# Kernel tuning notes

Measured on AMD Instinct MI355X. Metric: run time of the kernel, lower is better.

## Reference

```python
import jax, jax.numpy as jnp
import numpy as np

V = 4096      # num codes (vocab)
D = 128       # embedding dim
K = 3         # diffusion scales
H = 4         # attn heads
FF = 128      # ff hidden
L = 2         # attn layers
NVIS = 8192   # visits
MAXC = 32     # max codes per visit
PAD = 0


def logmap0(x):
    # Poincare ball (c=1) log map at origin: artanh(||x||) * x / ||x||
    eps = 1e-7
    norm = jnp.linalg.norm(x, axis=-1, keepdims=True)
    norm_c = jnp.clip(norm, eps, 1.0 - 1e-5)
    return jnp.arctanh(norm_c) * x / jnp.maximum(norm, eps)


def layer_norm(x, g, b, eps=1e-5):
    m = jnp.mean(x, axis=-1, keepdims=True)
    v = jnp.mean((x - m) ** 2, axis=-1, keepdims=True)
    return (x - m) * jax.lax.rsqrt(v + eps) * g + b


def attn_block(x, Wqkv, bqkv, Wo, bo, W1, b1, W2, b2, g1, be1, g2, be2):
    # x: [V, D] (batch of 1, squeezed)
    hd = D // H
    qkv = x @ Wqkv.T + bqkv                      # [V, 3D]
    q, k, v = jnp.split(qkv, 3, axis=-1)
    q = q.reshape(V, H, hd)
    k = k.reshape(V, H, hd)
    v = v.reshape(V, H, hd)
    scores = jnp.einsum('shd,thd->hst', q, k) / np.sqrt(hd).astype(x.dtype)
    a = jax.nn.softmax(scores, axis=-1)          # [H, V, V]
    o = jnp.einsum('hst,thd->shd', a, v).reshape(V, D)
    attn_out = o @ Wo.T + bo
    x = layer_norm(x + attn_out, g1, be1)
    ff = jax.nn.gelu(x @ W1.T + b1) @ W2.T + b2
    return layer_norm(x + ff, g2, be2)


def setup_inputs() -> dict:
    key = jax.random.key(0)
    ks = jax.random.split(key, 20)
    inp = {}
    inp['visits'] = jax.random.randint(ks[0], (NVIS, MAXC), 0, V)
    # hyperbolic points inside unit ball
    inp['X_hyp'] = jax.random.normal(ks[1], (V, D), jnp.float32) * 0.01
    inp['kernels'] = jax.random.normal(ks[2], (K, V, V), jnp.float32) / V
    inp['proj_W'] = jax.random.normal(ks[3], (D, K * D), jnp.float32) * 0.05
    inp['proj_b'] = jnp.zeros((D,), jnp.float32)
    s = 0.05
    inp['Wqkv'] = jax.random.normal(ks[4], (L, 3 * D, D), jnp.float32) * s
    inp['bqkv'] = jnp.zeros((L, 3 * D), jnp.float32)
    inp['Wo'] = jax.random.normal(ks[5], (L, D, D), jnp.float32) * s
    inp['bo'] = jnp.zeros((L, D), jnp.float32)
    inp['W1'] = jax.random.normal(ks[6], (L, FF, D), jnp.float32) * s
    inp['b1'] = jnp.zeros((L, FF), jnp.float32)
    inp['W2'] = jax.random.normal(ks[7], (L, D, FF), jnp.float32) * s
    inp['b2'] = jnp.zeros((L, D), jnp.float32)
    inp['ln1_g'] = jnp.ones((L, D), jnp.float32)
    inp['ln1_b'] = jnp.zeros((L, D), jnp.float32)
    inp['ln2_g'] = jnp.ones((L, D), jnp.float32)
    inp['ln2_b'] = jnp.zeros((L, D), jnp.float32)
    return inp


def reference(visits, X_hyp, kernels, proj_W, proj_b, Wqkv, bqkv, Wo, bo,
              W1, b1, W2, b2, ln1_g, ln1_b, ln2_g, ln2_b):
    # ---- hyperbolic graph diffusion ----
    Z0 = logmap0(X_hyp)                              # [V, D]
    Z_scales = jnp.einsum('kuv,vd->ukd', kernels, Z0)  # [V, K, D]
    Z_cat = Z_scales.reshape(V, K * D)
    H_ = Z_cat @ proj_W.T + proj_b                   # [V, D]
    # ---- global self-attention stack ----
    for l in range(L):
        H_ = attn_block(H_, Wqkv[l], bqkv[l], Wo[l], bo[l],
                        W1[l], b1[l], W2[l], b2[l],
                        ln1_g[l], ln1_b[l], ln2_g[l], ln2_b[l])
    # ---- per-visit masked mean pooling (segment mean) ----
    mask = (visits != PAD)                           # [NVIS, MAXC]
    gathered = H_[visits] * mask[..., None]          # [NVIS, MAXC, D]
    cnt = jnp.sum(mask, axis=-1, keepdims=True).astype(H_.dtype)
    summed = jnp.sum(gathered, axis=1)               # [NVIS, D]
    return jnp.where(cnt > 0, summed / jnp.maximum(cnt, 1.0), 0.0)
```

## Files before the change

### kernel.cpp

```cpp
#include <hip/hip_runtime.h>
#include <hip/hip_bf16.h>
#include <math.h>

#define VN 4096
#define DIM 128
#define KS 3
#define NH 4
#define HD 32
#define NVIS 8192
#define MAXC 32
#define KTOT (KS*VN)
#define PITCH 136

typedef unsigned short u16;
typedef __attribute__((ext_vector_type(8))) short short8;
typedef __attribute__((ext_vector_type(4))) float f32x4;
typedef __attribute__((ext_vector_type(4))) float f4v;

__device__ __forceinline__ u16 f2b(float f){
  union { float f; unsigned u; } c; c.f = f;
  unsigned u = c.u;
  return (u16)((u + 0x7fffu + ((u >> 16) & 1u)) >> 16);
}
__device__ __forceinline__ float b2f(u16 x){
  union { float f; unsigned u; } c; c.u = ((unsigned)x) << 16; return c.f;
}
__device__ __forceinline__ unsigned cvt2(float lo, float hi){
  unsigned r;
  asm("v_cvt_pk_bf16_f32 %0, %1, %2" : "=v"(r) : "v"(lo), "v"(hi));
  return r;
}
#define MFMA16(a,b,c) __builtin_amdgcn_mfma_f32_16x16x32_bf16((a),(b),(c),0,0,0)

__global__ __launch_bounds__(256) void k_wprep(const float* __restrict__ Wqkv, const float* __restrict__ Wo,
                                               const float* __restrict__ W1, const float* __restrict__ W2,
                                               u16* __restrict__ wb){
  int t = blockIdx.x*256 + threadIdx.x;
  #pragma unroll
  for(int i=0;i<2;i++){
    int e = t + 24576*i;
    const float* s; u16* d; int ge;
    if(e < 24576){ s = Wqkv; d = wb;          ge = e; }
    else if(e < 32768){ s = Wo; d = wb + 98304;  ge = e - 24576; }
    else if(e < 40960){ s = W1; d = wb + 131072; ge = e - 32768; }
    else              { s = W2; d = wb + 163840; ge = e - 40960; }
    float4 f = *(const float4*)&s[(size_t)ge*4];
    uint2 o = { cvt2(f.x,f.y), cvt2(f.z,f.w) };
    *(uint2*)&d[(size_t)ge*4] = o;
  }
}

__global__ __launch_bounds__(256) void k_logmap(const float* __restrict__ xh, u16* __restrict__ z0){
  __shared__ float xs[64][132];
  __shared__ float part[4][64];
  __shared__ float sscale[64];
  int t = threadIdx.x;
  int v0 = blockIdx.x * 64;
  #pragma unroll
  for(int i=0;i<8;i++){
    int id = t + 256*i; int e = id*4; int r = e>>7; int c = e&127;
    float4 u = *(const float4*)&xh[(size_t)(v0+r)*DIM + c];
    xs[r][c+0]=u.x; xs[r][c+1]=u.y; xs[r][c+2]=u.z; xs[r][c+3]=u.w;
  }
  __syncthreads();
  int r = t & 63, q = t >> 6;
  float p = 0.f;
  #pragma unroll
  for(int c=0;c<32;c++){ float x = xs[r][q*32+c]; p += x*x; }
  part[q][r] = p;
  __syncthreads();
  if(t < 64){
    float ss = part[0][t]+part[1][t]+part[2][t]+part[3][t];
    float n = sqrtf(ss);
    float nc = fminf(fmaxf(n, 1e-7f), 1.0f - 1e-5f);
    sscale[t] = atanhf(nc) / fmaxf(n, 1e-7f);
  }
  __syncthreads();
  #pragma unroll
  for(int i=0;i<8;i++){
    int id = t + 256*i; int e = id*4; int rr = e>>7; int cc = e&127;
    float s = sscale[rr];
    uint2 o = { cvt2(xs[rr][cc+0]*s, xs[rr][cc+1]*s),
                cvt2(xs[rr][cc+2]*s, xs[rr][cc+3]*s) };
    *(uint2*)&z0[(size_t)(v0+rr)*DIM + cc] = o;
  }
}

template<bool AF32, bool BF32>
__device__ __forceinline__ void gemm_k128_t(const void* __restrict__ Agv, int lda,
                                            const void* __restrict__ Bgv, int ldb,
                                            u16 (*As)[128*72], u16 (*Bs)[128*72], f32x4 (&acc)[2][8]){
  int t = threadIdx.x;
  int w=t>>6, lane=t&63, l15=lane&15, quad=lane>>4;
  #pragma unroll
  for(int s=0;s<2;s++)
    #pragma unroll
    for(int n=0;n<8;n++) acc[s][n] = (f32x4){0.f,0.f,0.f,0.f};

  float4 af[4][2]; uint4 ai[4];
  float4 bf[4][2]; uint4 bi[4];

  auto LOAD = [&](int kb){
    #pragma unroll
    for(int i=0;i<4;i++){
      int id = t + 256*i; int row = id>>3, c8 = id&7;
      if constexpr(AF32){
        const float* Ag = (const float*)Agv;
        af[i][0] = *(const float4*)&Ag[(size_t)row*lda + kb + c8*8];
        af[i][1] = *(const float4*)&Ag[(size_t)row*lda + kb + c8*8 + 4];
      } else {
        const u16* Ag = (const u16*)Agv;
        ai[i] = *(const uint4*)&Ag[(size_t)row*lda + kb + c8*8];
      }
      if constexpr(BF32){
        const float* Bg = (const float*)Bgv;
        bf[i][0] = *(const float4*)&Bg[(size_t)row*ldb + kb + c8*8];
        bf[i][1] = *(const float4*)&Bg[(size_t)row*ldb + kb + c8*8 + 4];
      } else {
        const u16* Bg = (const u16*)Bgv;
        bi[i] = *(const uint4*)&Bg[(size_t)row*ldb + kb + c8*8];
      }
    }
  };
  auto COMMIT = [&](u16* Ad, u16* Bd){
    #pragma unroll
    for(int i=0;i<4;i++){
      int id = t + 256*i; int row = id>>3, c8 = id&7;
      if constexpr(AF32){
        uint4 p = { cvt2(af[i][0].x, af[i][0].y), cvt2(af[i][0].z, af[i][0].w),
                    cvt2(af[i][1].x, af[i][1].y), cvt2(af[i][1].z, af[i][1].w) };
        *(uint4*)&Ad[row*72 + c8*8] = p;
      } else {
        *(uint4*)&Ad[row*72 + c8*8] = ai[i];
      }
      if constexpr(BF32){
        uint4 q = { cvt2(bf[i][0].x, bf[i][0].y), cvt2(bf[i][0].z, bf[i][0].w),
                    cvt2(bf[i][1].x, bf[i][1].y), cvt2(bf[i][1].z, bf[i][1].w) };
        *(uint4*)&Bd[row*72 + c8*8] = q;
      } else {
        *(uint4*)&Bd[row*72 + c8*8] = bi[i];
      }
    }
  };
  auto COMPUTE = [&](const u16* Asb, const u16* Bsb){
    #pragma unroll
    for(int ks=0; ks<2; ks++){
      short8 a[2], b[8];
      #pragma unroll
      for(int s=0;s<2;s++) a[s] = *(const short8*)&Asb[(w*32+s*16+l15)*72 + (ks*4+quad)*8];
      #pragma unroll
      for(int n=0;n<8;n++)  b[n] = *(const short8*)&Bsb[(n*16+l15)*72 + (ks*4+quad)*8];
      #pragma unroll
      for(int s=0;s<2;s++)
        #pragma unroll
        for(int n=0;n<8;n++) acc[s][n] = MFMA16(a[s], b[n], acc[s][n]);
    }
  };

  LOAD(0);  COMMIT(As[0], Bs[0]);  __syncthreads();
  LOAD(64); COMPUTE(As[0], Bs[0]); COMMIT(As[1], Bs[1]); __syncthreads();
  COMPUTE(As[1], Bs[1]);
}

__global__ __launch_bounds__(256) void k_gproj(const float* __restrict__ projW, const u16* __restrict__ z0,
                                               u16* __restrict__ gbuf){
  __shared__ u16 As[2][128*72], Bs[2][128*72];
  int kb = blockIdx.x >> 5, vt = blockIdx.x & 31;
  f32x4 acc[2][8];
  gemm_k128_t<true,false>(projW + kb*128, 3*DIM, z0 + (size_t)vt*128*DIM, DIM, As, Bs, acc);
  int t=threadIdx.x, w=t>>6, lane=t&63, l15=lane&15, quad=lane>>4;
  #pragma unroll
  for(int s=0;s<2;s++)
    #pragma unroll
    for(int n=0;n<8;n++)
      #pragma unroll
      for(int rg=0;rg<4;rg++){
        int d = w*32 + s*16 + quad*4 + rg;
        int v = vt*128 + n*16 + l15;
        gbuf[(size_t)(d*KS + kb)*VN + v] = f2b(acc[s][n][rg]);
      }
}

__global__ __launch_bounds__(256) void k_diff(const float* __restrict__ kers, const u16* __restrict__ gbuf,
                                              u16* __restrict__ hpart){
  __shared__ u16 As[2][128*72], Bs[2][128*72];
  int t = threadIdx.x;
  int mt = blockIdx.x & 31;
  int sl = blockIdx.x >> 5;
  int w=t>>6, lane=t&63, l15=lane&15, quad=lane>>4;
  f32x4 acc[2][8];
  #pragma unroll
  for(int s=0;s<2;s++)
    #pragma unroll
    for(int n=0;n<8;n++) acc[s][n] = (f32x4){0.f,0.f,0.f,0.f};
  int k0 = sl * 768;

  f4v  fa0[4], fa1[4];
  uint4 fb[4];

  auto LOADSTEP = [&](int step){
    int kk = k0 + step*64;
    int kout = kk >> 12; int vv = kk & 4095;
    #pragma unroll
    for(int i=0;i<4;i++){
      int id = t + 256*i; int row = id>>3, c8 = id&7;
      const float* ap = &kers[((size_t)kout<<24) + (size_t)(mt*128+row)*VN + vv + c8*8];
      fa0[i] = __builtin_nontemporal_load((const f4v*)ap);
      fa1[i] = __builtin_nontemporal_load((const f4v*)(ap+4));
      fb[i]  = *(const uint4*)&gbuf[(size_t)row*KTOT + kk + c8*8];
    }
  };
  auto COMMIT = [&](u16* Ad, u16* Bd){
    #pragma unroll
    for(int i=0;i<4;i++){
      int id = t + 256*i; int row = id>>3, c8 = id&7;
      uint4 pa = { cvt2(fa0[i].x, fa0[i].y), cvt2(fa0[i].z, fa0[i].w),
                   cvt2(fa1[i].x, fa1[i].y), cvt2(fa1[i].z, fa1[i].w) };
      *(uint4*)&Ad[row*72 + c8*8] = pa;
      *(uint4*)&Bd[row*72 + c8*8] = fb[i];
    }
  };
  auto COMPUTE = [&](const u16* Asb, const u16* Bsb){
    #pragma unroll
    for(int ks=0; ks<2; ks++){
      short8 a[2], b[8];
      #pragma unroll
      for(int s=0;s<2;s++) a[s] = *(const short8*)&Asb[(w*32+s*16+l15)*72 + (ks*4+quad)*8];
      #pragma unroll
      for(int n=0;n<8;n++)  b[n] = *(const short8*)&Bsb[(n*16+l15)*72 + (ks*4+quad)*8];
      #pragma unroll
      for(int s=0;s<2;s++)
        #pragma unroll
        for(int n=0;n<8;n++) acc[s][n] = MFMA16(a[s], b[n], acc[s][n]);
    }
  };

  LOADSTEP(0);
  COMMIT(As[0], Bs[0]);
  __syncthreads();
  #pragma unroll 1
  for(int sp=0; sp<6; sp++){
    LOADSTEP(2*sp+1);
    COMPUTE(As[0], Bs[0]);
    COMMIT(As[1], Bs[1]);
    __syncthreads();
    if(sp < 5){
      LOADSTEP(2*sp+2);
      COMPUTE(As[1], Bs[1]);
      COMMIT(As[0], Bs[0]);
      __syncthreads();
    }
  }
  COMPUTE(As[1], Bs[1]);

  u16* dst = hpart + ((size_t)blockIdx.x << 14);
  #pragma unroll
  for(int s=0;s<2;s++)
    #pragma unroll
    for(int n=0;n<8;n++)
      #pragma unroll
      for(int rg=0;rg<4;rg++)
        dst[(w*32+s*16+quad*4+rg)*128 + n*16 + l15] = f2b(acc[s][n][rg]);
}

__global__ __launch_bounds__(256) void k_hreduce(const u16* __restrict__ hpart, const float* __restrict__ pb,
                                                 float* __restrict__ h0){
  int idx = blockIdx.x*256 + threadIdx.x;
  int e0 = idx*4;
  int c0 = e0 & 127;
  float4 r;
  r.x = pb[c0+0]; r.y = pb[c0+1]; r.z = pb[c0+2]; r.w = pb[c0+3];
  #pragma unroll
  for(int sl=0; sl<16; sl++){
    uint2 u = *(const uint2*)&hpart[((size_t)sl<<19) + e0];
    r.x += b2f((u16)(u.x & 0xffffu)); r.y += b2f((u16)(u.x >> 16));
    r.z += b2f((u16)(u.y & 0xffffu)); r.w += b2f((u16)(u.y >> 16));
  }
  *(float4*)&h0[e0] = r;
}

__device__ __forceinline__ void sg_stageB(const u16* __restrict__ wb, u16* Bs){
  int t = threadIdx.x;
  #pragma unroll
  for(int i=0;i<16;i++){
    int e = t + 128*i; int row = e>>4, c16 = e&15;
    *(uint4*)&Bs[row*PITCH + c16*8] = *(const uint4*)&wb[row*128 + c16*8];
  }
}
__device__ __forceinline__ void sg_stageA_b(const u16* __restrict__ src, int m0, u16* As){
  int t = threadIdx.x;
  #pragma unroll
  for(int i=0;i<4;i++){
    int e = t + 128*i; int row = e>>4, c16 = e&15;
    *(uint4*)&As[row*PITCH + c16*8] = *(const uint4*)&src[(size_t)(m0+row)*DIM + c16*8];
  }
}
__device__ __forceinline__ void sg_stageA_f(const float* __restrict__ src, int m0, u16* As){
  int t = threadIdx.x;
  #pragma unroll
  for(int i=0;i<8;i++){
    int e = t + 128*i; int row = e>>5, c4 = e&31;
    float4 f = *(const float4*)&src[(size_t)(m0+row)*DIM + c4*4];
    uint2 o = { cvt2(f.x,f.y), cvt2(f.z,f.w) };
    *(uint2*)&As[row*PITCH + c4*4] = o;
  }
}
__device__ __forceinline__ void sg_compute(const u16* As, const u16* Bs, f32x4 (&acc)[8]){
  int t=threadIdx.x, w=t>>6, lane=t&63, l15=lane&15, quad=lane>>4;
  #pragma unroll
  for(int n=0;n<8;n++) acc[n] = (f32x4){0.f,0.f,0.f,0.f};
  #pragma unroll
  for(int kk=0;kk<4;kk++){
    short8 a = *(const short8*)&As[(w*16+l15)*PITCH + kk*32 + quad*8];
    #pragma unroll
    for(int n=0;n<8;n++){
      short8 b = *(const short8*)&Bs[(n*16+l15)*PITCH + kk*32 + quad*8];
      acc[n] = MFMA16(a, b, acc[n]);
    }
  }
}
__device__ __forceinline__ void sg_ln(f32x4 (&acc)[8], const float* __restrict__ g,
                                      const float* __restrict__ bv, int l15){
  #pragma unroll
  for(int rg=0;rg<4;rg++){
    float a=0.f, bs=0.f;
    #pragma unroll
    for(int n=0;n<8;n++){ float x = acc[n][rg]; a += x; bs += x*x; }
    #pragma unroll
    for(int off=1;off<16;off<<=1){ a += __shfl_xor(a, off, 64); bs += __shfl_xor(bs, off, 64); }
    float mean = a*(1.f/128.f);
    float var  = bs*(1.f/128.f) - mean*mean;
    float rstd = rsqrtf(var + 1e-5f);
    #pragma unroll
    for(int n=0;n<8;n++){
      int col = n*16 + l15;
      acc[n][rg] = (acc[n][rg] - mean)*rstd*g[col] + bv[col];
    }
  }
}

template<bool AF32>
__global__ __launch_bounds__(128) void k_qkv_s(const void* __restrict__ xb, const u16* __restrict__ wq,
                                               const float* __restrict__ bq, u16* __restrict__ outq){
  __shared__ u16 As[32*PITCH], Bs[128*PITCH];
  int bx = blockIdx.x; int mt = bx & 127, nt = bx >> 7;
  if(AF32) sg_stageA_f((const float*)xb, mt*32, As);
  else     sg_stageA_b((const u16*)xb, mt*32, As);
  sg_stageB(wq + nt*16384, Bs);
  __syncthreads();
  f32x4 acc[8]; sg_compute(As, Bs, acc);
  int t=threadIdx.x, w=t>>6, lane=t&63, l15=lane&15, quad=lane>>4;
  #pragma unroll
  for(int n=0;n<8;n++)
    #pragma unroll
    for(int rg=0;rg<4;rg++){
      int row = mt*32 + w*16 + quad*4 + rg;
      int col = nt*128 + n*16 + l15;
      outq[(size_t)row*(3*DIM) + col] = f2b(acc[n][rg] + bq[col]);
    }
}

__global__ __launch_bounds__(128) void k_oprojln_s(const float* __restrict__ opart, const float* __restrict__ mlpart,
                                                   const u16* __restrict__ wo,
                                                   const float* __restrict__ bias, const float* __restrict__ resf,
                                                   const float* __restrict__ g, const float* __restrict__ bb,
                                                   float* __restrict__ outf, u16* __restrict__ outb){
  __shared__ u16 As[32*PITCH], Bs[128*PITCH];
  int mt = blockIdx.x; int t = threadIdx.x;
  #pragma unroll
  for(int i=0;i<8;i++){
    int e = t + 128*i; int row = e>>5, c4 = e&31; int col = c4*4;
    int hh = col>>5, c0 = col&31;
    int grow = mt*32 + row;
    int hq = hh*64 + (grow>>6); int rr = grow & 63;
    const float* o0  = opart  + ((size_t)(hq*2)   << 11);
    const float* o1  = opart  + ((size_t)(hq*2+1) << 11);
    const float* ml0 = mlpart + ((size_t)(hq*2)   << 7);
    const float* ml1 = mlpart + ((size_t)(hq*2+1) << 7);
    float m0 = ml0[rr], l0 = ml0[64+rr], m1 = ml1[rr], l1 = ml1[64+rr];
    float m = fmaxf(m0, m1);
    float w0 = __expf(m0 - m), w1 = __expf(m1 - m);
    float inv = 1.f / (l0*w0 + l1*w1);
    float4 a  = *(const float4*)&o0[rr*32 + c0];
    float4 c  = *(const float4*)&o1[rr*32 + c0];
    uint2 o = { cvt2((a.x*w0+c.x*w1)*inv, (a.y*w0+c.y*w1)*inv),
                cvt2((a.z*w0+c.z*w1)*inv, (a.w*w0+c.w*w1)*inv) };
    *(uint2*)&As[row*PITCH + col] = o;
  }
  sg_stageB(wo, Bs);
  __syncthreads();
  f32x4 acc[8]; sg_compute(As, Bs, acc);
  int w=t>>6, lane=t&63, l15=lane&15, quad=lane>>4;
  #pragma unroll
  for(int n=0;n<8;n++)
    #pragma unroll
    for(int rg=0;rg<4;rg++){
      int row = mt*32 + w*16 + quad*4 + rg;
      int col = n*16 + l15;
      acc[n][rg] += bias[col] + resf[(size_t)row*DIM + col];
    }
  sg_ln(acc, g, bb, l15);
  #pragma unroll
  for(int n=0;n<8;n++)
    #pragma unroll
    for(int rg=0;rg<4;rg++){
      int row = mt*32 + w*16 + quad*4 + rg;
      int col = n*16 + l15;
      float y = acc[n][rg];
      outf[(size_t)row*DIM + col] = y;
      outb[(size_t)row*DIM + col] = f2b(y);
    }
}

__global__ __launch_bounds__(128) void k_ff1_s(const u16* __restrict__ Ab, const u16* __restrict__ w1,
                                               const float* __restrict__ bias, u16* __restrict__ outb){
  __shared__ u16 As[32*PITCH], Bs[128*PITCH];
  int mt = blockIdx.x;
  sg_stageA_b(Ab, mt*32, As);
  sg_stageB(w1, Bs);
  __syncthreads();
  f32x4 acc[8]; sg_compute(As, Bs, acc);
  int t=threadIdx.x, w=t>>6, lane=t&63, l15=lane&15, quad=lane>>4;
  #pragma unroll
  for(int n=0;n<8;n++)
    #pragma unroll
    for(int rg=0;rg<4;rg++){
      int row = mt*32 + w*16 + quad*4 + rg;
      int col = n*16 + l15;
      float v = acc[n][rg] + bias[col];
      float z = 0.7978845608028654f*(v + 0.044715f*v*v*v);
      float e = __expf(2.f*z);
      float th = 1.f - 2.f/(e + 1.f);
      outb[(size_t)row*DIM + col] = f2b(0.5f*v*(1.f + th));
    }
}

__global__ __launch_bounds__(128) void k_projln_s(const u16* __restrict__ Ab, const u16* __restrict__ w2,
                                                  const float* __restrict__ bias, const float* __restrict__ resf,
                                                  const float* __restrict__ g, const float* __restrict__ bb,
                                                  float* __restrict__ outf, u16* __restrict__ outb){
  __shared__ u16 As[32*PITCH], Bs[128*PITCH];
  int mt = blockIdx.x;
  sg_stageA_b(Ab, mt*32, As);
  sg_stageB(w2, Bs);
  __syncthreads();
  f32x4 acc[8]; sg_compute(As, Bs, acc);
  int t=threadIdx.x, w=t>>6, lane=t&63, l15=lane&15, quad=lane>>4;
  #pragma unroll
  for(int n=0;n<8;n++)
    #pragma unroll
    for(int rg=0;rg<4;rg++){
      int row = mt*32 + w*16 + quad*4 + rg;
      int col = n*16 + l15;
      acc[n][rg] += bias[col] + resf[(size_t)row*DIM + col];
    }
  sg_ln(acc, g, bb, l15);
  #pragma unroll
  for(int n=0;n<8;n++)
    #pragma unroll
    for(int rg=0;rg<4;rg++){
      int row = mt*32 + w*16 + quad*4 + rg;
      int col = n*16 + l15;
      float y = acc[n][rg];
      outf[(size_t)row*DIM + col] = y;
      outb[(size_t)row*DIM + col] = f2b(y);
    }
}

__global__ __launch_bounds__(256) void k_attn(const u16* __restrict__ qkv, float* __restrict__ opart,
                                              float* __restrict__ mlpart){
  __shared__ u16 Qs[64*40];
  __shared__ u16 Ksh[2][128*40];
  __shared__ u16 Vt[2][32*136];
  __shared__ u16 Ps[4*16*136];
  int t=threadIdx.x;
  int b = blockIdx.x;
  int h = b>>7, qt = (b>>1)&63, half = b&1;
  int w=t>>6, lane=t&63, l15=lane&15, quad=lane>>4;
  { int r = t>>2, c = t&3;
    *(uint4*)&Qs[r*40 + c*8] = *(const uint4*)&qkv[(size_t)(qt*64+r)*(3*DIM) + h*HD + c*8];
  }
  int skey = t>>2, sc4 = t&3;
  uint4 kreg[2], vreg[2];
  #pragma unroll
  for(int i=0;i<2;i++){
    int key = skey + 64*i;
    kreg[i] = *(const uint4*)&qkv[(size_t)((size_t)(half*16)*128+key)*(3*DIM) + DIM + h*HD + sc4*8];
    vreg[i] = *(const uint4*)&qkv[(size_t)((size_t)(half*16)*128+key)*(3*DIM) + 2*DIM + h*HD + sc4*8];
  }
  #pragma unroll
  for(int i=0;i<2;i++){
    int key = skey + 64*i;
    *(uint4*)&Ksh[0][key*40 + sc4*8] = kreg[i];
    u16 tmp[8]; *(uint4*)tmp = vreg[i];
    #pragma unroll
    for(int j=0;j<8;j++) Vt[0][(sc4*8+j)*136 + key] = tmp[j];
  }
  __syncthreads();
  short8 aq = *(short8*)&Qs[(w*16+l15)*40 + quad*8];
  f32x4 oacc[2]; oacc[0]=(f32x4){0.f,0.f,0.f,0.f}; oacc[1]=(f32x4){0.f,0.f,0.f,0.f};
  float mrun[4], lrun[4];
  #pragma unroll
  for(int rg=0;rg<4;rg++){ mrun[rg] = -INFINITY; lrun[rg] = 0.f; }
  const float sc = 0.17677669529663687f;
  for(int kti=0;kti<16;kti++){
    int cur = kti&1;
    if(kti<15){
      int kt = half*16 + kti + 1;
      #pragma unroll
      for(int i=0;i<2;i++){
        int key = skey + 64*i;
        kreg[i] = *(const uint4*)&qkv[(size_t)(kt*128+key)*(3*DIM) + DIM + h*HD + sc4*8];
        vreg[i] = *(const uint4*)&qkv[(size_t)(kt*128+key)*(3*DIM) + 2*DIM + h*HD + sc4*8];
      }
    }
    f32x4 s[8];
    #pragma unroll
    for(int n=0;n<8;n++)
      s[n] = MFMA16(aq, *(short8*)&Ksh[cur][(n*16+l15)*40 + quad*8], ((f32x4){0.f,0.f,0.f,0.f}));
    float mx[4];
    #pragma unroll
    for(int rg=0;rg<4;rg++){
      float m = -INFINITY;
      #pragma unroll
      for(int n=0;n<8;n++) m = fmaxf(m, s[n][rg]);
      #pragma unroll
      for(int off=1;off<16;off<<=1) m = fmaxf(m, __shfl_xor(m, off, 64));
      mx[rg] = m;
    }
    bool grew = false;
    #pragma unroll
    for(int rg=0;rg<4;rg++) grew = grew || (mx[rg] > mrun[rg]);
    if(__any(grew)){
      #pragma unroll
      for(int rg=0;rg<4;rg++){
        float mn = fmaxf(mrun[rg], mx[rg]);
        float alpha = __expf(sc*(mrun[rg] - mn));
        mrun[rg] = mn;
        lrun[rg] *= alpha;
        oacc[0][rg] *= alpha; oacc[1][rg] *= alpha;
      }
    }
    float rs[4];
    #pragma unroll
    for(int rg=0;rg<4;rg++) rs[rg] = 0.f;
    #pragma unroll
    for(int n=0;n<8;n++)
      #pragma unroll
      for(int rg=0;rg<4;rg++){
        float p = __expf(sc*(s[n][rg] - mrun[rg]));
        s[n][rg] = p; rs[rg] += p;
      }
    #pragma unroll
    for(int rg=0;rg<4;rg++){
      #pragma unroll
      for(int off=1;off<16;off<<=1) rs[rg] += __shfl_xor(rs[rg], off, 64);
      lrun[rg] += rs[rg];
    }
    #pragma unroll
    for(int n=0;n<8;n++)
      #pragma unroll
      for(int rg=0;rg<4;rg++)
        Ps[w*16*136 + (quad*4+rg)*136 + n*16 + l15] = f2b(s[n][rg]);
    #pragma unroll
    for(int kt2=0;kt2<4;kt2++){
      short8 ap = *(short8*)&Ps[w*16*136 + l15*136 + kt2*32 + quad*8];
      #pragma unroll
      for(int n2=0;n2<2;n2++)
        oacc[n2] = MFMA16(ap, *(short8*)&Vt[cur][(n2*16+l15)*136 + kt2*32 + quad*8], oacc[n2]);
    }
    if(kti<15){
      #pragma unroll
      for(int i=0;i<2;i++){
        int key = skey + 64*i;
        *(uint4*)&Ksh[cur^1][key*40 + sc4*8] = kreg[i];
        u16 tmp[8]; *(uint4*)tmp = vreg[i];
        #pragma unroll
        for(int j=0;j<8;j++) Vt[cur^1][(sc4*8+j)*136 + key] = tmp[j];
      }
    }
    __syncthreads();
  }
  float* op = opart + ((size_t)b << 11);
  #pragma unroll
  for(int n2=0;n2<2;n2++)
    #pragma unroll
    for(int rg=0;rg<4;rg++)
      op[(w*16+quad*4+rg)*32 + n2*16 + l15] = oacc[n2][rg];
  if(l15 == 0){
    float* ml = mlpart + ((size_t)b << 7);
    #pragma unroll
    for(int rg=0;rg<4;rg++){
      int r = w*16 + quad*4 + rg;
      ml[r] = sc*mrun[rg]; ml[64 + r] = lrun[rg];
    }
  }
}

__global__ __launch_bounds__(256) void k_pool(const int* __restrict__ visits, const float* __restrict__ xf,
                                              float* __restrict__ out){
  int t = threadIdx.x;
  int vis = blockIdx.x*2 + (t>>7);
  int col = t & 127;
  float s = 0.f; int cnt = 0;
  #pragma unroll
  for(int j=0;j<MAXC;j++){
    int idx = visits[vis*MAXC + j];
    if(idx != 0){ s += xf[(size_t)idx*DIM + col]; cnt++; }
  }
  float r = (cnt > 0) ? s/(float)cnt : 0.f;
  out[(size_t)vis*DIM + col] = r;
}

extern "C" void kernel_launch(void* const* d_in, const int* in_sizes, int n_in,
                              void* d_out, int out_size, void* d_ws, size_t ws_size,
                              hipStream_t stream){
  (void)in_sizes; (void)n_in; (void)out_size; (void)ws_size;
  const int*   visits = (const int*)d_in[0];
  const float* xhyp  = (const float*)d_in[1];
  const float* kers  = (const float*)d_in[2];
  const float* projW = (const float*)d_in[3];
  const float* projb = (const float*)d_in[4];
  const float* Wqkv  = (const float*)d_in[5];
  const float* bqkv  = (const float*)d_in[6];
  const float* Wo    = (const float*)d_in[7];
  const float* bo    = (const float*)d_in[8];
  const float* W1    = (const float*)d_in[9];
  const float* b1    = (const float*)d_in[10];
  const float* W2    = (const float*)d_in[11];
  const float* b2    = (const float*)d_in[12];
  const float* g1    = (const float*)d_in[13];
  const float* be1   = (const float*)d_in[14];
  const float* g2    = (const float*)d_in[15];
  const float* be2   = (const float*)d_in[16];

  char* ws = (char*)d_ws;
  u16*   z0    = (u16*)(ws);
  u16*   gbuf  = (u16*)(ws + (1u<<20));
  float* h0    = (float*)(ws + (4u<<20));
  u16*   qkvb  = (u16*)(ws + (7u<<20));
  float* ln1f  = (float*)(ws + (11u<<20));
  u16*   ln1b  = (u16*)(ws + (13u<<20));
  u16*   ffa   = (u16*)(ws + (14u<<20));
  float* x1f   = (float*)(ws + (15u<<20));
  u16*   x1b   = (u16*)(ws + (17u<<20));
  float* x2f   = (float*)(ws + (18u<<20));
  u16*   x2b   = (u16*)(ws + (20u<<20));
  u16*   hpart = (u16*)(ws + (21u<<20));
  u16*   wb    = (u16*)(ws + (40u<<20));
  float* opart = (float*)(ws + (53u<<20));
  float* mlprt = (float*)(ws + (57u<<20));

  k_wprep<<<96,256,0,stream>>>(Wqkv, Wo, W1, W2, wb);
  k_logmap<<<64,256,0,stream>>>(xhyp, z0);
  k_gproj<<<96,256,0,stream>>>(projW, z0, gbuf);
  k_diff<<<512,256,0,stream>>>(kers, gbuf, hpart);
  k_hreduce<<<512,256,0,stream>>>(hpart, projb, h0);

  const u16* wq_l[2] = { wb,            wb + 49152 };
  const u16* wo_l[2] = { wb + 98304,    wb + 98304 + 16384 };
  const u16* w1_l[2] = { wb + 131072,   wb + 131072 + 16384 };
  const u16* w2_l[2] = { wb + 163840,   wb + 163840 + 16384 };

  k_qkv_s<true><<<384,128,0,stream>>>((const void*)h0, wq_l[0], bqkv, qkvb);
  k_attn<<<512,256,0,stream>>>(qkvb, opart, mlprt);
  k_oprojln_s<<<128,128,0,stream>>>(opart, mlprt, wo_l[0], bo, h0, g1, be1, ln1f, ln1b);
  k_ff1_s<<<128,128,0,stream>>>(ln1b, w1_l[0], b1, ffa);
  k_projln_s<<<128,128,0,stream>>>(ffa, w2_l[0], b2, ln1f, g2, be2, x1f, x1b);
  k_qkv_s<false><<<384,128,0,stream>>>((const void*)x1b, wq_l[1], bqkv + 3*DIM, qkvb);
  k_attn<<<512,256,0,stream>>>(qkvb, opart, mlprt);
  k_oprojln_s<<<128,128,0,stream>>>(opart, mlprt, wo_l[1], bo + DIM, x1f, g1 + DIM, be1 + DIM, ln1f, ln1b);
  k_ff1_s<<<128,128,0,stream>>>(ln1b, w1_l[1], b1 + DIM, ffa);
  k_projln_s<<<128,128,0,stream>>>(ffa, w2_l[1], b2 + DIM, ln1f, g2 + DIM, be2 + DIM, x2f, x2b);

  k_pool<<<4096,256,0,stream>>>(visits, x2f, (float*)d_out);
}
```

Baseline: 527.7 us.

## Fuse per-layer post-attention GEMMs and QKV into single-wave kernels

Merges weight conversion with the logmap kernel, fuses the diffusion partial reduction into the first QKV projection, and collapses out-proj+LN, FF1+GELU, FF2+LN and the next layer's QKV into one kernel per layer. Each block becomes a single 64-thread wave handling 16 rows, so LDS barriers are dropped and intermediate activations stay in registers or LDS rather than being written to and re-read from global memory. This cuts kernel launches and round-trips through global memory. In exchange, each block stages several weight matrices serially with little latency hiding, and overall occupancy and parallelism per launch are lower.

Measured after the change: 618.1 us. 17.1% more time.

```diff
diff --git a/kernel.cpp b/kernel.cpp
--- a/kernel.cpp
+++ b/kernel.cpp
@@ -32,29 +32,30 @@
 }
 #define MFMA16(a,b,c) __builtin_amdgcn_mfma_f32_16x16x32_bf16((a),(b),(c),0,0,0)
 
-__global__ __launch_bounds__(256) void k_wprep(const float* __restrict__ Wqkv, const float* __restrict__ Wo,
-                                               const float* __restrict__ W1, const float* __restrict__ W2,
-                                               u16* __restrict__ wb){
-  int t = blockIdx.x*256 + threadIdx.x;
-  #pragma unroll
-  for(int i=0;i<2;i++){
-    int e = t + 24576*i;
-    const float* s; u16* d; int ge;
-    if(e < 24576){ s = Wqkv; d = wb;          ge = e; }
-    else if(e < 32768){ s = Wo; d = wb + 98304;  ge = e - 24576; }
-    else if(e < 40960){ s = W1; d = wb + 131072; ge = e - 32768; }
-    else              { s = W2; d = wb + 163840; ge = e - 40960; }
-    float4 f = *(const float4*)&s[(size_t)ge*4];
-    uint2 o = { cvt2(f.x,f.y), cvt2(f.z,f.w) };
-    *(uint2*)&d[(size_t)ge*4] = o;
-  }
-}
-
-__global__ __launch_bounds__(256) void k_logmap(const float* __restrict__ xh, u16* __restrict__ z0){
+__global__ __launch_bounds__(256) void k_prep(const float* __restrict__ xh, u16* __restrict__ z0,
+                                              const float* __restrict__ Wqkv, const float* __restrict__ Wo,
+                                              const float* __restrict__ W1, const float* __restrict__ W2,
+                                              u16* __restrict__ wb){
   __shared__ float xs[64][132];
   __shared__ float part[4][64];
   __shared__ float sscale[64];
   int t = threadIdx.x;
+  if(blockIdx.x >= 64){
+    int gt = (blockIdx.x - 64)*256 + t;
+    #pragma unroll
+    for(int i=0;i<2;i++){
+      int e = gt + 24576*i;
+      const float* s; u16* d; int ge;
+      if(e < 24576){ s = Wqkv; d = wb;          ge = e; }
+      else if(e < 32768){ s = Wo; d = wb + 98304;  ge = e - 24576; }
+      else if(e < 40960){ s = W1; d = wb + 131072; ge = e - 32768; }
+      else              { s = W2; d = wb + 163840; ge = e - 40960; }
+      float4 f = *(const float4*)&s[(size_t)ge*4];
+      uint2 o = { cvt2(f.x,f.y), cvt2(f.z,f.w) };
+      *(uint2*)&d[(size_t)ge*4] = o;
+    }
+    return;
+  }
   int v0 = blockIdx.x * 64;
   #pragma unroll
   for(int i=0;i<8;i++){
@@ -263,55 +264,21 @@
         dst[(w*32+s*16+quad*4+rg)*128 + n*16 + l15] = f2b(acc[s][n][rg]);
 }
 
-__global__ __launch_bounds__(256) void k_hreduce(const u16* __restrict__ hpart, const float* __restrict__ pb,
-                                                 float* __restrict__ h0){
-  int idx = blockIdx.x*256 + threadIdx.x;
-  int e0 = idx*4;
-  int c0 = e0 & 127;
-  float4 r;
-  r.x = pb[c0+0]; r.y = pb[c0+1]; r.z = pb[c0+2]; r.w = pb[c0+3];
-  #pragma unroll
-  for(int sl=0; sl<16; sl++){
-    uint2 u = *(const uint2*)&hpart[((size_t)sl<<19) + e0];
-    r.x += b2f((u16)(u.x & 0xffffu)); r.y += b2f((u16)(u.x >> 16));
-    r.z += b2f((u16)(u.y & 0xffffu)); r.w += b2f((u16)(u.y >> 16));
-  }
-  *(float4*)&h0[e0] = r;
-}
-
-__device__ __forceinline__ void sg_stageB(const u16* __restrict__ wb, u16* Bs){
+__device__ __forceinline__ void sg64_stageB(const u16* __restrict__ wb, u16* Bs){
   int t = threadIdx.x;
   #pragma unroll
-  for(int i=0;i<16;i++){
-    int e = t + 128*i; int row = e>>4, c16 = e&15;
+  for(int i=0;i<32;i++){
+    int e = t + 64*i; int row = e>>4, c16 = e&15;
     *(uint4*)&Bs[row*PITCH + c16*8] = *(const uint4*)&wb[row*128 + c16*8];
   }
 }
-__device__ __forceinline__ void sg_stageA_b(const u16* __restrict__ src, int m0, u16* As){
-  int t = threadIdx.x;
-  #pragma unroll
-  for(int i=0;i<4;i++){
-    int e = t + 128*i; int row = e>>4, c16 = e&15;
-    *(uint4*)&As[row*PITCH + c16*8] = *(const uint4*)&src[(size_t)(m0+row)*DIM + c16*8];
-  }
-}
-__device__ __forceinline__ void sg_stageA_f(const float* __restrict__ src, int m0, u16* As){
-  int t = threadIdx.x;
-  #pragma unroll
-  for(int i=0;i<8;i++){
-    int e = t + 128*i; int row = e>>5, c4 = e&31;
-    float4 f = *(const float4*)&src[(size_t)(m0+row)*DIM + c4*4];
-    uint2 o = { cvt2(f.x,f.y), cvt2(f.z,f.w) };
-    *(uint2*)&As[row*PITCH + c4*4] = o;
-  }
-}
-__device__ __forceinline__ void sg_compute(const u16* As, const u16* Bs, f32x4 (&acc)[8]){
-  int t=threadIdx.x, w=t>>6, lane=t&63, l15=lane&15, quad=lane>>4;
+__device__ __forceinline__ void sg64_compute(const u16* As, const u16* Bs, f32x4 (&acc)[8]){
+  int lane=threadIdx.x&63, l15=lane&15, quad=lane>>4;
   #pragma unroll
   for(int n=0;n<8;n++) acc[n] = (f32x4){0.f,0.f,0.f,0.f};
   #pragma unroll
   for(int kk=0;kk<4;kk++){
-    short8 a = *(const short8*)&As[(w*16+l15)*PITCH + kk*32 + quad*8];
+    short8 a = *(const short8*)&As[l15*PITCH + kk*32 + quad*8];
     #pragma unroll
     for(int n=0;n<8;n++){
       short8 b = *(const short8*)&Bs[(n*16+l15)*PITCH + kk*32 + quad*8];
@@ -319,8 +286,8 @@
     }
   }
 }
-__device__ __forceinline__ void sg_ln(f32x4 (&acc)[8], const float* __restrict__ g,
-                                      const float* __restrict__ bv, int l15){
+__device__ __forceinline__ void sg64_ln(f32x4 (&acc)[8], const float* __restrict__ g,
+                                        const float* __restrict__ bv, int l15){
   #pragma unroll
   for(int rg=0;rg<4;rg++){
     float a=0.f, bs=0.f;
@@ -338,40 +305,71 @@
     }
   }
 }
-
-template<bool AF32>
-__global__ __launch_bounds__(128) void k_qkv_s(const void* __restrict__ xb, const u16* __restrict__ wq,
-                                               const float* __restrict__ bq, u16* __restrict__ outq){
-  __shared__ u16 As[32*PITCH], Bs[128*PITCH];
-  int bx = blockIdx.x; int mt = bx & 127, nt = bx >> 7;
-  if(AF32) sg_stageA_f((const float*)xb, mt*32, As);
-  else     sg_stageA_b((const u16*)xb, mt*32, As);
-  sg_stageB(wq + nt*16384, Bs);
-  __syncthreads();
-  f32x4 acc[8]; sg_compute(As, Bs, acc);
-  int t=threadIdx.x, w=t>>6, lane=t&63, l15=lane&15, quad=lane>>4;
+__device__ __forceinline__ void sg64_writeA(f32x4 (&y)[8], u16* As, int l15, int quad){
   #pragma unroll
   for(int n=0;n<8;n++)
     #pragma unroll
-    for(int rg=0;rg<4;rg++){
-      int row = mt*32 + w*16 + quad*4 + rg;
-      int col = nt*128 + n*16 + l15;
-      outq[(size_t)row*(3*DIM) + col] = f2b(acc[n][rg] + bq[col]);
-    }
-}
-
-__global__ __launch_bounds__(128) void k_oprojln_s(const float* __restrict__ opart, const float* __restrict__ mlpart,
-                                                   const u16* __restrict__ wo,
-                                                   const float* __restrict__ bias, const float* __restrict__ resf,
-                                                   const float* __restrict__ g, const float* __restrict__ bb,
-                                                   float* __restrict__ outf, u16* __restrict__ outb){
-  __shared__ u16 As[32*PITCH], Bs[128*PITCH];
-  int mt = blockIdx.x; int t = threadIdx.x;
+    for(int rg=0;rg<4;rg++)
+      As[(quad*4+rg)*PITCH + n*16 + l15] = f2b(y[n][rg]);
+}
+
+__global__ __launch_bounds__(64) void k_hqkv(const u16* __restrict__ hpart, const float* __restrict__ pb,
+                                             const u16* __restrict__ wq, const float* __restrict__ bq,
+                                             float* __restrict__ h0, u16* __restrict__ outq){
+  __shared__ u16 As[16*PITCH], Bs[128*PITCH];
+  int mt = blockIdx.x;
+  int t = threadIdx.x, lane=t&63, l15=lane&15, quad=lane>>4;
   #pragma unroll
   for(int i=0;i<8;i++){
-    int e = t + 128*i; int row = e>>5, c4 = e&31; int col = c4*4;
+    int e = t + 64*i; int row = e>>5, c4 = e&31;
+    int ge = (mt*16+row)*DIM + c4*4;
+    int c0 = c4*4;
+    float4 r;
+    r.x = pb[c0+0]; r.y = pb[c0+1]; r.z = pb[c0+2]; r.w = pb[c0+3];
+    #pragma unroll
+    for(int sl=0; sl<16; sl++){
+      uint2 u = *(const uint2*)&hpart[((size_t)sl<<19) + ge];
+      r.x += b2f((u16)(u.x & 0xffffu)); r.y += b2f((u16)(u.x >> 16));
+      r.z += b2f((u16)(u.y & 0xffffu)); r.w += b2f((u16)(u.y >> 16));
+    }
+    *(float4*)&h0[ge] = r;
+    uint2 o = { cvt2(r.x,r.y), cvt2(r.z,r.w) };
+    *(uint2*)&As[row*PITCH + c0] = o;
+  }
+  #pragma unroll 1
+  for(int nt=0; nt<3; nt++){
+    sg64_stageB(wq + nt*16384, Bs);
+    f32x4 acc[8]; sg64_compute(As, Bs, acc);
+    #pragma unroll
+    for(int n=0;n<8;n++)
+      #pragma unroll
+      for(int rg=0;rg<4;rg++){
+        int row = mt*16 + quad*4 + rg;
+        int col = nt*128 + n*16 + l15;
+        outq[(size_t)row*(3*DIM) + col] = f2b(acc[n][rg] + bq[col]);
+      }
+  }
+}
+
+template<bool QKV>
+__global__ __launch_bounds__(64) void k_layer(const float* __restrict__ opart, const float* __restrict__ mlpart,
+                                              const u16* __restrict__ wo, const float* __restrict__ bo,
+                                              const float* __restrict__ resf,
+                                              const float* __restrict__ g1, const float* __restrict__ be1,
+                                              const u16* __restrict__ w1, const float* __restrict__ b1,
+                                              const u16* __restrict__ w2, const float* __restrict__ b2,
+                                              const float* __restrict__ g2, const float* __restrict__ be2,
+                                              float* __restrict__ outf,
+                                              const u16* __restrict__ wq, const float* __restrict__ bq,
+                                              u16* __restrict__ qkvout){
+  __shared__ u16 As[16*PITCH], Bs[128*PITCH];
+  int mt = blockIdx.x;
+  int t = threadIdx.x, lane=t&63, l15=lane&15, quad=lane>>4;
+  #pragma unroll
+  for(int i=0;i<8;i++){
+    int e = t + 64*i; int row = e>>5, c4 = e&31; int col = c4*4;
     int hh = col>>5, c0 = col&31;
-    int grow = mt*32 + row;
+    int grow = mt*16 + row;
     int hq = hh*64 + (grow>>6); int rr = grow & 63;
     const float* o0  = opart  + ((size_t)(hq*2)   << 11);
     const float* o1  = opart  + ((size_t)(hq*2+1) << 11);
@@ -379,92 +377,77 @@
     const float* ml1 = mlpart + ((size_t)(hq*2+1) << 7);
     float m0 = ml0[rr], l0 = ml0[64+rr], m1 = ml1[rr], l1 = ml1[64+rr];
     float m = fmaxf(m0, m1);
-    float w0 = __expf(m0 - m), w1 = __expf(m1 - m);
-    float inv = 1.f / (l0*w0 + l1*w1);
+    float w0 = __expf(m0 - m), w1f = __expf(m1 - m);
+    float inv = 1.f / (l0*w0 + l1*w1f);
     float4 a  = *(const float4*)&o0[rr*32 + c0];
     float4 c  = *(const float4*)&o1[rr*32 + c0];
-    uint2 o = { cvt2((a.x*w0+c.x*w1)*inv, (a.y*w0+c.y*w1)*inv),
-                cvt2((a.z*w0+c.z*w1)*inv, (a.w*w0+c.w*w1)*inv) };
+    uint2 o = { cvt2((a.x*w0+c.x*w1f)*inv, (a.y*w0+c.y*w1f)*inv),
+                cvt2((a.z*w0+c.z*w1f)*inv, (a.w*w0+c.w*w1f)*inv) };
     *(uint2*)&As[row*PITCH + col] = o;
   }
-  sg_stageB(wo, Bs);
-  __syncthreads();
-  f32x4 acc[8]; sg_compute(As, Bs, acc);
-  int w=t>>6, lane=t&63, l15=lane&15, quad=lane>>4;
+  sg64_stageB(wo, Bs);
+  f32x4 acc[8]; sg64_compute(As, Bs, acc);
   #pragma unroll
   for(int n=0;n<8;n++)
     #pragma unroll
     for(int rg=0;rg<4;rg++){
-      int row = mt*32 + w*16 + quad*4 + rg;
+      int row = mt*16 + quad*4 + rg;
       int col = n*16 + l15;
-      acc[n][rg] += bias[col] + resf[(size_t)row*DIM + col];
-    }
-  sg_ln(acc, g, bb, l15);
+      acc[n][rg] += bo[col] + resf[(size_t)row*DIM + col];
+    }
+  sg64_ln(acc, g1, be1, l15);
+  f32x4 y1[8];
+  #pragma unroll
+  for(int n=0;n<8;n++) y1[n] = acc[n];
+  sg64_writeA(y1, As, l15, quad);
+  sg64_stageB(w1, Bs);
+  sg64_compute(As, Bs, acc);
   #pragma unroll
   for(int n=0;n<8;n++)
     #pragma unroll
     for(int rg=0;rg<4;rg++){
-      int row = mt*32 + w*16 + quad*4 + rg;
       int col = n*16 + l15;
-      float y = acc[n][rg];
-      outf[(size_t)row*DIM + col] = y;
-      outb[(size_t)row*DIM + col] = f2b(y);
-    }
-}
-
-__global__ __launch_bounds__(128) void k_ff1_s(const u16* __restrict__ Ab, const u16* __restrict__ w1,
-                                               const float* __restrict__ bias, u16* __restrict__ outb){
-  __shared__ u16 As[32*PITCH], Bs[128*PITCH];
-  int mt = blockIdx.x;
-  sg_stageA_b(Ab, mt*32, As);
-  sg_stageB(w1, Bs);
-  __syncthreads();
-  f32x4 acc[8]; sg_compute(As, Bs, acc);
-  int t=threadIdx.x, w=t>>6, lane=t&63, l15=lane&15, quad=lane>>4;
-  #pragma unroll
-  for(int n=0;n<8;n++)
-    #pragma unroll
-    for(int rg=0;rg<4;rg++){
-      int row = mt*32 + w*16 + quad*4 + rg;
-      int col = n*16 + l15;
-      float v = acc[n][rg] + bias[col];
+      float v = acc[n][rg] + b1[col];
       float z = 0.7978845608028654f*(v + 0.044715f*v*v*v);
       float e = __expf(2.f*z);
       float th = 1.f - 2.f/(e + 1.f);
-      outb[(size_t)row*DIM + col] = f2b(0.5f*v*(1.f + th));
-    }
-}
-
-__global__ __launch_bounds__(128) void k_projln_s(const u16* __restrict__ Ab, const u16* __restrict__ w2,
-                                                  const float* __restrict__ bias, const float* __restrict__ resf,
-                                                  const float* __restrict__ g, const float* __restrict__ bb,
-                                                  float* __restrict__ outf, u16* __restrict__ outb){
-  __shared__ u16 As[32*PITCH], Bs[128*PITCH];
-  int mt = blockIdx.x;
-  sg_stageA_b(Ab, mt*32, As);
-  sg_stageB(w2, Bs);
-  __syncthreads();
-  f32x4 acc[8]; sg_compute(As, Bs, acc);
-  int t=threadIdx.x, w=t>>6, lane=t&63, l15=lane&15, quad=lane>>4;
+      acc[n][rg] = 0.5f*v*(1.f + th);
+    }
+  sg64_writeA(acc, As, l15, quad);
+  sg64_stageB(w2, Bs);
+  sg64_compute(As, Bs, acc);
   #pragma unroll
   for(int n=0;n<8;n++)
     #pragma unroll
     for(int rg=0;rg<4;rg++){
-      int row = mt*32 + w*16 + quad*4 + rg;
       int col = n*16 + l15;
-      acc[n][rg] += bias[col] + resf[(size_t)row*DIM + col];
-    }
-  sg_ln(acc, g, bb, l15);
+      acc[n][rg] += b2[col] + y1[n][rg];
+    }
+  sg64_ln(acc, g2, be2, l15);
   #pragma unroll
   for(int n=0;n<8;n++)
     #pragma unroll
     for(int rg=0;rg<4;rg++){
-      int row = mt*32 + w*16 + quad*4 + rg;
+      int row = mt*16 + quad*4 + rg;
       int col = n*16 + l15;
-      float y = acc[n][rg];
-      outf[(size_t)row*DIM + col] = y;
-      outb[(size_t)row*DIM + col] = f2b(y);
-    }
+      outf[(size_t)row*DIM + col] = acc[n][rg];
+    }
+  if constexpr(QKV){
+    sg64_writeA(acc, As, l15, quad);
+    #pragma unroll 1
+    for(int nt=0; nt<3; nt++){
+      sg64_stageB(wq + nt*16384, Bs);
+      f32x4 acc2[8]; sg64_compute(As, Bs, acc2);
+      #pragma unroll
+      for(int n=0;n<8;n++)
+        #pragma unroll
+        for(int rg=0;rg<4;rg++){
+          int row = mt*16 + quad*4 + rg;
+          int col = nt*128 + n*16 + l15;
+          qkvout[(size_t)row*(3*DIM) + col] = f2b(acc2[n][rg] + bq[col]);
+        }
+    }
+  }
 }
 
 __global__ __launch_bounds__(256) void k_attn(const u16* __restrict__ qkv, float* __restrict__ opart,
@@ -639,39 +622,31 @@
   u16*   gbuf  = (u16*)(ws + (1u<<20));
   float* h0    = (float*)(ws + (4u<<20));
   u16*   qkvb  = (u16*)(ws + (7u<<20));
-  float* ln1f  = (float*)(ws + (11u<<20));
-  u16*   ln1b  = (u16*)(ws + (13u<<20));
-  u16*   ffa   = (u16*)(ws + (14u<<20));
   float* x1f   = (float*)(ws + (15u<<20));
-  u16*   x1b   = (u16*)(ws + (17u<<20));
   float* x2f   = (float*)(ws + (18u<<20));
-  u16*   x2b   = (u16*)(ws + (20u<<20));
   u16*   hpart = (u16*)(ws + (21u<<20));
   u16*   wb    = (u16*)(ws + (40u<<20));
   float* opart = (float*)(ws + (53u<<20));
   float* mlprt = (float*)(ws + (57u<<20));
 
-  k_wprep<<<96,256,0,stream>>>(Wqkv, Wo, W1, W2, wb);
-  k_logmap<<<64,256,0,stream>>>(xhyp, z0);
+  k_prep<<<160,256,0,stream>>>(xhyp, z0, Wqkv, Wo, W1, W2, wb);
   k_gproj<<<96,256,0,stream>>>(projW, z0, gbuf);
   k_diff<<<512,256,0,stream>>>(kers, gbuf, hpart);
-  k_hreduce<<<512,256,0,stream>>>(hpart, projb, h0);
 
   const u16* wq_l[2] = { wb,            wb + 49152 };
   const u16* wo_l[2] = { wb + 98304,    wb + 98304 + 16384 };
   const u16* w1_l[2] = { wb + 131072,   wb + 131072 + 16384 };
   const u16* w2_l[2] = { wb + 163840,   wb + 163840 + 16384 };
 
-  k_qkv_s<true><<<384,128,0,stream>>>((const void*)h0, wq_l[0], bqkv, qkvb);
+  k_hqkv<<<256,64,0,stream>>>(hpart, projb, wq_l[0], bqkv, h0, qkvb);
   k_attn<<<512,256,0,stream>>>(qkvb, opart, mlprt);
-  k_oprojln_s<<<128,128,0,stream>>>(opart, mlprt, wo_l[0], bo, h0, g1, be1, ln1f, ln1b);
-  k_ff1_s<<<128,128,0,stream>>>(ln1b, w1_l[0], b1, ffa);
-  k_projln_s<<<128,128,0,stream>>>(ffa, w2_l[0], b2, ln1f, g2, be2, x1f, x1b);
-  k_qkv_s<false><<<384,128,0,stream>>>((const void*)x1b, wq_l[1], bqkv + 3*DIM, qkvb);
+  k_layer<true><<<256,64,0,stream>>>(opart, mlprt, wo_l[0], bo, h0, g1, be1,
+                                     w1_l[0], b1, w2_l[0], b2, g2, be2, x1f,
+                                     wq_l[1], bqkv + 3*DIM, qkvb);
   k_attn<<<512,256,0,stream>>>(qkvb, opart, mlprt);
-  k_oprojln_s<<<128,128,0,stream>>>(opart, mlprt, wo_l[1], bo + DIM, x1f, g1 + DIM, be1 + DIM, ln1f, ln1b);
-  k_ff1_s<<<128,128,0,stream>>>(ln1b, w1_l[1], b1 + DIM, ffa);
-  k_projln_s<<<128,128,0,stream>>>(ffa, w2_l[1], b2 + DIM, ln1f, g2 + DIM, be2 + DIM, x2f, x2b);
-
+  k_layer<false><<<256,64,0,stream>>>(opart, mlprt, wo_l[1], bo + DIM, x1f,
+                                      g1 + DIM, be1 + DIM, w1_l[1], b1 + DIM,
+                                      w2_l[1], b2 + DIM, g2 + DIM, be2 + DIM, x2f,
+                                      nullptr, nullptr, nullptr);
   k_pool<<<4096,256,0,stream>>>(visits, x2f, (float*)d_out);
 }
```
